# Kernel optimization log

Hardware: AMD Instinct MI355X
Metric: run time of the kernel (lower is better)

The kernel has to match this reference:

```python
import jax, jax.numpy as jnp
import numpy as np

NG, NC, D, E, L, OUT = 100000, 2000, 256, 1000000, 2, 64


def setup_inputs() -> dict:
    key = jax.random.key(0)
    ks = jax.random.split(key, 16)
    s = 1.0 / np.sqrt(D)
    return dict(
        x_gene=jax.random.normal(ks[0], (NG, D), dtype=jnp.float32),
        x_cell=jax.random.normal(ks[1], (NC, D), dtype=jnp.float32),
        src_g2c=jax.random.randint(ks[2], (E,), 0, NG),
        dst_g2c=jax.random.randint(ks[3], (E,), 0, NC),
        src_c2g=jax.random.randint(ks[4], (E,), 0, NC),
        dst_c2g=jax.random.randint(ks[5], (E,), 0, NG),
        idx_gg=jnp.arange(NG),
        idx_cc=jnp.arange(NC),
        w_g2c=jax.random.uniform(ks[6], (E,), dtype=jnp.float32),
        w_c2g=jax.random.uniform(ks[7], (E,), dtype=jnp.float32),
        w_gg=jax.random.uniform(ks[8], (NG,), dtype=jnp.float32),
        w_cc=jax.random.uniform(ks[9], (NC,), dtype=jnp.float32),
        Wrel=jax.random.normal(ks[10], (L, 4, D, D), dtype=jnp.float32) * s,
        brel=jax.random.normal(ks[11], (L, 4, D), dtype=jnp.float32) * 0.1,
        Wroot=jax.random.normal(ks[12], (L, 4, D, D), dtype=jnp.float32) * s,
        Wout=jax.random.normal(ks[13], (OUT, D), dtype=jnp.float32) * s,
        bout=jax.random.normal(ks[14], (OUT,), dtype=jnp.float32) * 0.1,
    )


def _agg(x_src, src, dst, w, n_dst):
    # GraphConv message: x_j * edge_weight, then scatter-add to destinations
    msg = x_src[src] * w[:, None]  # [E, D]
    return jax.ops.segment_sum(msg, dst, num_segments=n_dst)


def reference(x_gene, x_cell, src_g2c, dst_g2c, src_c2g, dst_c2g,
              idx_gg, idx_cc, w_g2c, w_c2g, w_gg, w_cc,
              Wrel, brel, Wroot, Wout, bout):
    xg, xc = x_gene, x_cell
    for l in range(L):
        # relation 0: gene -> cell_type; 1: cell_type -> gene;
        # relation 2: gene self-loop; 3: cell_type self-loop
        agg_c = _agg(xg, src_g2c, dst_g2c, w_g2c, NC)
        agg_g = _agg(xc, src_c2g, dst_c2g, w_c2g, NG)
        agg_gg = _agg(xg, idx_gg, idx_gg, w_gg, NG)
        agg_cc = _agg(xc, idx_cc, idx_cc, w_cc, NC)
        # GraphConv: lin_rel(agg) + bias + lin_root(x_dst); HeteroConv aggr='sum'
        new_c = (agg_c @ Wrel[l, 0].T + brel[l, 0] + xc @ Wroot[l, 0].T
                 + agg_cc @ Wrel[l, 3].T + brel[l, 3] + xc @ Wroot[l, 3].T)
        new_g = (agg_g @ Wrel[l, 1].T + brel[l, 1] + xg @ Wroot[l, 1].T
                 + agg_gg @ Wrel[l, 2].T + brel[l, 2] + xg @ Wroot[l, 2].T)
        xg, xc = jax.nn.relu(new_g), jax.nn.relu(new_c)
    return xc @ Wout.T + bout  # [NC, OUT]
```

## Files before the change

### kernel.cpp

```cpp
#include <hip/hip_runtime.h>

static constexpr int NG   = 100000;
static constexpr int NC   = 2000;
static constexpr int D    = 256;
static constexpr int NE   = 1000000;
static constexpr int NOUTD= 64;
static constexpr int KCAT = 768;

typedef __bf16 bf16x8 __attribute__((ext_vector_type(8)));
typedef float  f32x4  __attribute__((ext_vector_type(4)));

__device__ __forceinline__ unsigned short f2bf(float f) {
    unsigned u = __float_as_uint(f);
    u += 0x7fffu + ((u >> 16) & 1u);
    return (unsigned short)(u >> 16);
}
__device__ __forceinline__ float bflo(unsigned x) { return __uint_as_float((x & 0xffffu) << 16); }
__device__ __forceinline__ float bfhi(unsigned x) { return __uint_as_float(x & 0xffff0000u); }

__device__ __forceinline__ void async16(const void* g, void* l) {
    __builtin_amdgcn_global_load_lds(
        (const __attribute__((address_space(1))) void*)g,
        (__attribute__((address_space(3))) void*)l, 16, 0, 0);
}

__global__ void prep_x(const float* __restrict__ x, const float* __restrict__ w,
                       unsigned short* __restrict__ dx, unsigned short* __restrict__ dv,
                       long stride, int rows) {
    int i = blockIdx.x * blockDim.x + threadIdx.x;
    if (i >= rows * (D / 4)) return;
    int row = i >> 6, c4 = (i & 63) * 4;
    float4 xv = *reinterpret_cast<const float4*>(x + (size_t)row * D + c4);
    float wv = w[row];
    uint2 ox, ov;
    ox.x = (unsigned)f2bf(xv.x) | ((unsigned)f2bf(xv.y) << 16);
    ox.y = (unsigned)f2bf(xv.z) | ((unsigned)f2bf(xv.w) << 16);
    ov.x = (unsigned)f2bf(xv.x * wv) | ((unsigned)f2bf(xv.y * wv) << 16);
    ov.y = (unsigned)f2bf(xv.z * wv) | ((unsigned)f2bf(xv.w * wv) << 16);
    *reinterpret_cast<uint2*>(dx + (size_t)row * stride + c4) = ox;
    *reinterpret_cast<uint2*>(dv + (size_t)row * stride + c4) = ov;
}

__global__ void build_wcat3(const float* __restrict__ Wrel, const float* __restrict__ Wroot,
                            const float* __restrict__ brel,
                            unsigned short* __restrict__ Wg0, unsigned short* __restrict__ Wc0,
                            unsigned short* __restrict__ Wc1,
                            float* __restrict__ bg0, float* __restrict__ bc0,
                            float* __restrict__ bc1) {
    int i = blockIdx.x * blockDim.x + threadIdx.x;
    if (i >= D * D) return;
    int ia, ib; unsigned short* wout; float* bsum;
    if (blockIdx.y == 0)      { ia = 1; ib = 2; wout = Wg0; bsum = bg0; }
    else if (blockIdx.y == 1) { ia = 0; ib = 3; wout = Wc0; bsum = bc0; }
    else                      { ia = 4; ib = 7; wout = Wc1; bsum = bc1; }
    const int WW = D * D;
    int n = i >> 8, k = i & 255;
    wout[(size_t)n * KCAT + k]        = f2bf(Wrel[ia * WW + i]);
    wout[(size_t)n * KCAT + 256 + k]  = f2bf(Wroot[ia * WW + i] + Wroot[ib * WW + i]);
    wout[(size_t)n * KCAT + 512 + k]  = f2bf(Wrel[ib * WW + i]);
    if (i < D) bsum[i] = brel[ia * D + i] + brel[ib * D + i];
}

static constexpr int CC_CHUNK = 8192;
__global__ __launch_bounds__(256) void coarse_count(const int* __restrict__ dst_g2c,
                                                    const int* __restrict__ dst_c2g,
                                                    int* __restrict__ hist) {
    __shared__ int h[512];
    h[threadIdx.x] = 0; h[256 + threadIdx.x] = 0;
    __syncthreads();
    int base = blockIdx.x * CC_CHUNK;
#pragma unroll 4
    for (int t = 0; t < CC_CHUNK / 256; ++t) {
        int e = base + t * 256 + threadIdx.x;
        if (e < NE) {
            atomicAdd(&h[dst_g2c[e] >> 3], 1);
            atomicAdd(&h[256 + (dst_c2g[e] >> 9)], 1);
        }
    }
    __syncthreads();
    if (h[threadIdx.x]) atomicAdd(&hist[threadIdx.x], h[threadIdx.x]);
    if (h[256 + threadIdx.x]) atomicAdd(&hist[256 + threadIdx.x], h[256 + threadIdx.x]);
}

__global__ __launch_bounds__(256) void coarse_scan(const int* __restrict__ hist,
                                                   int* __restrict__ cbase,
                                                   int* __restrict__ ccur_c, int* __restrict__ ccur_g,
                                                   int* __restrict__ rp_c, int* __restrict__ rp_g) {
    __shared__ int sd[256];
    int t = threadIdx.x;
    {
        int v = hist[t];
        sd[t] = v; __syncthreads();
        for (int off = 1; off < 256; off <<= 1) {
            int u = (t >= off) ? sd[t - off] : 0; __syncthreads();
            sd[t] += u; __syncthreads();
        }
        int e = sd[t] - v;
        cbase[t] = e; ccur_c[t] = e;
        if (t == 255) cbase[256] = sd[255];
        __syncthreads();
    }
    {
        int v = hist[256 + t];
        sd[t] = v; __syncthreads();
        for (int off = 1; off < 256; off <<= 1) {
            int u = (t >= off) ? sd[t - off] : 0; __syncthreads();
            sd[t] += u; __syncthreads();
        }
        int e = sd[t] - v;
        cbase[257 + t] = e; ccur_g[t] = e;
        if (t == 255) cbase[513] = sd[255];
    }
    if (t == 0) { rp_c[NC] = NE; rp_g[NG] = NE; }
}

static constexpr int P1_CHUNK = 8192;
__global__ __launch_bounds__(256) void bucket_pass1(
        const int* __restrict__ srcA, const int* __restrict__ dstA, const float* __restrict__ wA,
        int* __restrict__ curA, int2* __restrict__ outA,
        const int* __restrict__ srcB, const int* __restrict__ dstB, const float* __restrict__ wB,
        int* __restrict__ curB, int2* __restrict__ outB) {
    __shared__ int hist[256], lcur[256], gbase[256];
    const int* src; const int* dst; const float* w; int* coarse_cur; int2* out;
    int shift, packshift;
    if (blockIdx.y == 0) { src = srcA; dst = dstA; w = wA; coarse_cur = curA; out = outA; shift = 3; packshift = 17; }
    else { src = srcB; dst = dstB; w = wB; coarse_cur = curB; out = outB; shift = 9; packshift = 11; }
    int tid = threadIdx.x;
    hist[tid] = 0;
    __syncthreads();
    int base = blockIdx.x * P1_CHUNK;
    int mybin[P1_CHUNK / 256];
#pragma unroll
    for (int t = 0; t < P1_CHUNK / 256; ++t) {
        int e = base + t * 256 + tid;
        if (e < NE) {
            int b = dst[e] >> shift;
            mybin[t] = b;
            atomicAdd(&hist[b], 1);
        } else mybin[t] = -1;
    }
    __syncthreads();
    int v = hist[tid];
    gbase[tid] = v ? atomicAdd(&coarse_cur[tid], v) : 0;
    lcur[tid] = 0;
    __syncthreads();
#pragma unroll
    for (int t = 0; t < P1_CHUNK / 256; ++t) {
        int b = mybin[t];
        if (b < 0) continue;
        int e = base + t * 256 + tid;
        int pos = gbase[b] + atomicAdd(&lcur[b], 1);
        int dl = dst[e] & ((1 << shift) - 1);
        out[pos] = make_int2(src[e] | (dl << packshift), __float_as_int(w[e]));
    }
}

static constexpr int P2_CBLK = NC / 8;
static constexpr int P2_GBLK = (NG + 511) / 512;
__global__ __launch_bounds__(256) void bucket_pass2(
        const int2* __restrict__ stC, int2* __restrict__ outC, int* __restrict__ rpC,
        const int2* __restrict__ stG, int2* __restrict__ outG, int* __restrict__ rpG,
        const int* __restrict__ cbase) {
    __shared__ int hist[512], cur[512], sd[256];
    const int2* staged; int2* out; int* rp; const int* cb;
    int shift, packshift, ndst, b;
    if (blockIdx.x < P2_CBLK) {
        staged = stC; out = outC; rp = rpC; cb = cbase;
        shift = 3; packshift = 17; ndst = NC; b = blockIdx.x;
    } else {
        staged = stG; out = outG; rp = rpG; cb = cbase + 257;
        shift = 9; packshift = 11; ndst = NG; b = blockIdx.x - P2_CBLK;
    }
    int tid = threadIdx.x;
    int nf = 1 << shift;
    int d0 = b << shift;
    int j0 = cb[b], j1 = cb[b + 1];
    for (int f = tid; f < nf; f += 256) hist[f] = 0;
    __syncthreads();
    for (int j = j0 + tid; j < j1; j += 256)
        atomicAdd(&hist[((unsigned)staged[j].x) >> packshift], 1);
    __syncthreads();
    int chunk = (nf + 255) >> 8;
    int s = 0;
#pragma unroll 2
    for (int k = 0; k < chunk; ++k) {
        int idx = tid * chunk + k;
        if (idx < nf) s += hist[idx];
    }
    sd[tid] = s; __syncthreads();
    for (int off = 1; off < 256; off <<= 1) {
        int u = (tid >= off) ? sd[tid - off] : 0; __syncthreads();
        sd[tid] += u; __syncthreads();
    }
    int run = sd[tid] - s;
#pragma unroll 2
    for (int k = 0; k < chunk; ++k) {
        int idx = tid * chunk + k;
        if (idx < nf) {
            int h = hist[idx];
            int pos = j0 + run;
            cur[idx] = pos;
            int d = d0 + idx;
            if (d < ndst) rp[d] = pos;
            run += h;
        }
    }
    __syncthreads();
    for (int j = j0 + tid; j < j1; j += 256) {
        int2 e = staged[j];
        int f = ((unsigned)e.x) >> packshift;
        int pos = atomicAdd(&cur[f], 1);
        out[pos] = make_int2(e.x & ((1 << packshift) - 1), e.y);
    }
}

__global__ __launch_bounds__(256) void sort_cell_edges(const int* __restrict__ rp,
                                                       int2* __restrict__ ec) {
    __shared__ int2 s[1024];
    int c = blockIdx.x;
    int j0 = rp[c], j1 = rp[c + 1];
    int n = j1 - j0;
    if (n <= 1 || n > 1024) return;
    for (int i = threadIdx.x; i < 1024; i += 256)
        s[i] = (i < n) ? ec[j0 + i] : make_int2(0x7fffffff, 0);
    __syncthreads();
    for (int k = 2; k <= 1024; k <<= 1) {
        for (int jj = k >> 1; jj > 0; jj >>= 1) {
#pragma unroll
            for (int t = 0; t < 4; ++t) {
                int i = threadIdx.x + t * 256;
                int ixj = i ^ jj;
                if (ixj > i) {
                    int2 a = s[i], b = s[ixj];
                    bool up = ((i & k) == 0);
                    if ((a.x > b.x) == up) { s[i] = b; s[ixj] = a; }
                }
            }
            __syncthreads();
        }
    }
    for (int i = threadIdx.x; i < n; i += 256) ec[j0 + i] = s[i];
}

__global__ void agg_gene_conv(const int* __restrict__ rp, const int2* __restrict__ eg,
                              const unsigned short* __restrict__ src, long sstride,
                              const float* __restrict__ x_gene,
                              unsigned short* __restrict__ xg0b,
                              unsigned short* __restrict__ agg_out, int nrows) {
    int wave = (blockIdx.x * blockDim.x + threadIdx.x) >> 6;
    int lane = threadIdx.x & 63;
    if (wave >= nrows) return;
    float4 xv = *reinterpret_cast<const float4*>(x_gene + (size_t)wave * D + lane * 4);
    uint2 xo;
    xo.x = (unsigned)f2bf(xv.x) | ((unsigned)f2bf(xv.y) << 16);
    xo.y = (unsigned)f2bf(xv.z) | ((unsigned)f2bf(xv.w) << 16);
    *reinterpret_cast<uint2*>(xg0b + (size_t)wave * D + lane * 4) = xo;
    int j0 = __builtin_amdgcn_readfirstlane(rp[wave]);
    int j1 = __builtin_amdgcn_readfirstlane(rp[wave + 1]);
    int half = lane >> 5;
    int lh = lane & 31;
    float a0=0.f,a1=0.f,a2=0.f,a3=0.f,a4=0.f,a5=0.f,a6=0.f,a7=0.f;
    int j = j0;
    for (; j + 4 <= j1; j += 4) {
        int2 e0 = eg[j], e1 = eg[j + 1], e2 = eg[j + 2], e3 = eg[j + 3];
        int   rA = half ? e1.x : e0.x;
        float wA = __int_as_float(half ? e1.y : e0.y);
        int   rB = half ? e3.x : e2.x;
        float wB = __int_as_float(half ? e3.y : e2.y);
        uint4 pA = *reinterpret_cast<const uint4*>(src + (size_t)rA * sstride + lh * 8);
        uint4 pB = *reinterpret_cast<const uint4*>(src + (size_t)rB * sstride + lh * 8);
        a0 += wA * bflo(pA.x) + wB * bflo(pB.x);
        a1 += wA * bfhi(pA.x) + wB * bfhi(pB.x);
        a2 += wA * bflo(pA.y) + wB * bflo(pB.y);
        a3 += wA * bfhi(pA.y) + wB * bfhi(pB.y);
        a4 += wA * bflo(pA.z) + wB * bflo(pB.z);
        a5 += wA * bfhi(pA.z) + wB * bfhi(pB.z);
        a6 += wA * bflo(pA.w) + wB * bflo(pB.w);
        a7 += wA * bfhi(pA.w) + wB * bfhi(pB.w);
    }
    for (; j < j1; j += 2) {
        int2 e0 = eg[j];
        int2 e1 = (j + 1 < j1) ? eg[j + 1] : make_int2(e0.x, 0);
        int   r = half ? e1.x : e0.x;
        float w = __int_as_float(half ? e1.y : e0.y);
        uint4 p = *reinterpret_cast<const uint4*>(src + (size_t)r * sstride + lh * 8);
        a0 += w * bflo(p.x); a1 += w * bfhi(p.x);
        a2 += w * bflo(p.y); a3 += w * bfhi(p.y);
        a4 += w * bflo(p.z); a5 += w * bfhi(p.z);
        a6 += w * bflo(p.w); a7 += w * bfhi(p.w);
    }
    a0 += __shfl_xor(a0, 32, 64); a1 += __shfl_xor(a1, 32, 64);
    a2 += __shfl_xor(a2, 32, 64); a3 += __shfl_xor(a3, 32, 64);
    a4 += __shfl_xor(a4, 32, 64); a5 += __shfl_xor(a5, 32, 64);
    a6 += __shfl_xor(a6, 32, 64); a7 += __shfl_xor(a7, 32, 64);
    if (lane < 32) {
        uint4 o;
        o.x = (unsigned)f2bf(a0) | ((unsigned)f2bf(a1) << 16);
        o.y = (unsigned)f2bf(a2) | ((unsigned)f2bf(a3) << 16);
        o.z = (unsigned)f2bf(a4) | ((unsigned)f2bf(a5) << 16);
        o.w = (unsigned)f2bf(a6) | ((unsigned)f2bf(a7) << 16);
        *reinterpret_cast<uint4*>(agg_out + (size_t)wave * D + lane * 8) = o;
    }
}

__global__ __launch_bounds__(256, 2) void gene_gemm(
        const unsigned short* __restrict__ Agg,
        const unsigned short* __restrict__ Xb,
        const float* __restrict__ w_gg,
        const unsigned short* __restrict__ W,
        const float* __restrict__ bias,
        unsigned short* __restrict__ xg1) {
    __shared__ unsigned short As[128 * 64];
    __shared__ unsigned short Bs1[128 * 64];
    __shared__ unsigned short Bs2[128 * 64];
    int tid = threadIdx.x;
    int wv = tid >> 6, ln = tid & 63;
    int lm = ln & 15, lq = ln >> 4;
    int m0 = blockIdx.x * 128;
    int nb = blockIdx.y * 128;
    int m0w = m0 + (wv >> 1) * 64;
    int n0w = nb + (wv & 1) * 64;

    f32x4 accA[4][4], accV[4][4];
#pragma unroll
    for (int i = 0; i < 4; ++i)
#pragma unroll
        for (int j = 0; j < 4; ++j) { accA[i][j] = f32x4{0,0,0,0}; accV[i][j] = f32x4{0,0,0,0}; }

    for (int k0 = 0; k0 < 256; k0 += 64) {
#pragma unroll
        for (int t = 0; t < 4; ++t) {
            int ci = t * 256 + tid;
            int r = ci >> 3, s = ci & 7;
            int cg = s ^ (r & 7);
            int row = m0 + r; if (row >= NG) row = NG - 1;
            async16(Agg + (size_t)row * D + k0 + cg * 8, (unsigned char*)As + ci * 16);
            async16(W + (size_t)(nb + r) * KCAT + k0 + cg * 8, (unsigned char*)Bs1 + ci * 16);
        }
        __syncthreads();
#pragma unroll
        for (int kk = 0; kk < 2; ++kk) {
            bf16x8 a[4], b[4];
#pragma unroll
            for (int i = 0; i < 4; ++i) {
                int r = (wv >> 1) * 64 + i * 16 + lm;
                int s = (kk * 4 + lq) ^ (r & 7);
                a[i] = *reinterpret_cast<const bf16x8*>(As + (r * 8 + s) * 8);
            }
#pragma unroll
            for (int j = 0; j < 4; ++j) {
                int r = (wv & 1) * 64 + j * 16 + lm;
                int s = (kk * 4 + lq) ^ (r & 7);
                b[j] = *reinterpret_cast<const bf16x8*>(Bs1 + (r * 8 + s) * 8);
            }
#pragma unroll
            for (int i = 0; i < 4; ++i)
#pragma unroll
                for (int j = 0; j < 4; ++j)
                    accA[i][j] = __builtin_amdgcn_mfma_f32_16x16x32_bf16(a[i], b[j], accA[i][j], 0, 0, 0);
        }
        __syncthreads();
    }

    for (int k0 = 0; k0 < 256; k0 += 64) {
#pragma unroll
        for (int t = 0; t < 4; ++t) {
            int ci = t * 256 + tid;
            int r = ci >> 3, s = ci & 7;
            int cg = s ^ (r & 7);
            int row = m0 + r; if (row >= NG) row = NG - 1;
            async16(Xb + (size_t)row * D + k0 + cg * 8, (unsigned char*)As + ci * 16);
            async16(W + (size_t)(nb + r) * KCAT + 256 + k0 + cg * 8, (unsigned char*)Bs1 + ci * 16);
            async16(W + (size_t)(nb + r) * KCAT + 512 + k0 + cg * 8, (unsigned char*)Bs2 + ci * 16);
        }
        __syncthreads();
#pragma unroll
        for (int kk = 0; kk < 2; ++kk) {
            bf16x8 a[4], b1[4], b2[4];
#pragma unroll
            for (int i = 0; i < 4; ++i) {
                int r = (wv >> 1) * 64 + i * 16 + lm;
                int s = (kk * 4 + lq) ^ (r & 7);
                a[i] = *reinterpret_cast<const bf16x8*>(As + (r * 8 + s) * 8);
            }
#pragma unroll
            for (int j = 0; j < 4; ++j) {
                int r = (wv & 1) * 64 + j * 16 + lm;
                int s = (kk * 4 + lq) ^ (r & 7);
                b1[j] = *reinterpret_cast<const bf16x8*>(Bs1 + (r * 8 + s) * 8);
                b2[j] = *reinterpret_cast<const bf16x8*>(Bs2 + (r * 8 + s) * 8);
            }
#pragma unroll
            for (int i = 0; i < 4; ++i)
#pragma unroll
                for (int j = 0; j < 4; ++j) {
                    accA[i][j] = __builtin_amdgcn_mfma_f32_16x16x32_bf16(a[i], b1[j], accA[i][j], 0, 0, 0);
                    accV[i][j] = __builtin_amdgcn_mfma_f32_16x16x32_bf16(a[i], b2[j], accV[i][j], 0, 0, 0);
                }
        }
        __syncthreads();
    }

#pragma unroll
    for (int i = 0; i < 4; ++i) {
#pragma unroll
        for (int r4 = 0; r4 < 4; ++r4) {
            int row = m0w + i * 16 + lq * 4 + r4;
            if (row >= NG) continue;
            float wr = w_gg[row];
#pragma unroll
            for (int j = 0; j < 4; ++j) {
                int col = n0w + j * 16 + lm;
                float v = accA[i][j][r4] + wr * accV[i][j][r4] + bias[col];
                v = v > 0.f ? v : 0.f;
                xg1[(size_t)row * D + col] = f2bf(v);
            }
        }
    }
}

__global__ __launch_bounds__(256) void agg_cell(const int* __restrict__ rp,
                                                const int2* __restrict__ ec,
                                                const unsigned short* __restrict__ src, long sstride,
                                                unsigned short* __restrict__ out, long ostride) {
    __shared__ float red[4][D];
    int c = blockIdx.x;
    int wv = threadIdx.x >> 6, ln = threadIdx.x & 63;
    int j0 = __builtin_amdgcn_readfirstlane(rp[c]);
    int j1 = __builtin_amdgcn_readfirstlane(rp[c + 1]);
    float a0 = 0.f, a1 = 0.f, a2 = 0.f, a3 = 0.f;
    int npair = (j1 - j0) & ~7;
    for (int j = j0 + wv * 2; j < j0 + npair; j += 8) {
        int2 e1 = ec[j], e2 = ec[j + 1];
        float w1 = __int_as_float(e1.y), w2 = __int_as_float(e2.y);
        uint2 p1 = *reinterpret_cast<const uint2*>(src + (size_t)e1.x * sstride + ln * 4);
        uint2 p2 = *reinterpret_cast<const uint2*>(src + (size_t)e2.x * sstride + ln * 4);
        a0 += w1 * bflo(p1.x) + w2 * bflo(p2.x);
        a1 += w1 * bfhi(p1.x) + w2 * bfhi(p2.x);
        a2 += w1 * bflo(p1.y) + w2 * bflo(p2.y);
        a3 += w1 * bfhi(p1.y) + w2 * bfhi(p2.y);
    }
    for (int j = j0 + npair + wv; j < j1; j += 4) {
        int2 e = ec[j];
        float w = __int_as_float(e.y);
        uint2 pk = *reinterpret_cast<const uint2*>(src + (size_t)e.x * sstride + ln * 4);
        a0 += w * bflo(pk.x); a1 += w * bfhi(pk.x);
        a2 += w * bflo(pk.y); a3 += w * bfhi(pk.y);
    }
    red[wv][ln * 4 + 0] = a0; red[wv][ln * 4 + 1] = a1;
    red[wv][ln * 4 + 2] = a2; red[wv][ln * 4 + 3] = a3;
    __syncthreads();
    int col = threadIdx.x;
    float s = red[0][col] + red[1][col] + red[2][col] + red[3][col];
    out[(size_t)c * ostride + col] = f2bf(s);
}

__global__ __launch_bounds__(256, 2) void gemm_tile(
        const unsigned short* __restrict__ A,
        const unsigned short* __restrict__ W,
        const float* __restrict__ bias,
        const float* __restrict__ wrow,
        unsigned short* __restrict__ xout, long xstride,
        unsigned short* __restrict__ vout,
        int M) {
    __shared__ unsigned short As[128 * 64];
    __shared__ unsigned short Bs[128 * 64];
    int tid = threadIdx.x;
    int wv = tid >> 6, ln = tid & 63;
    int lm = ln & 15, lq = ln >> 4;
    int m0 = blockIdx.x * 128;
    int nb = blockIdx.y * 128;
    int m0w = m0 + (wv >> 1) * 64;
    int n0w = nb + (wv & 1) * 64;

    f32x4 acc[4][4];
#pragma unroll
    for (int i = 0; i < 4; ++i)
#pragma unroll
        for (int j = 0; j < 4; ++j) acc[i][j] = f32x4{0.f, 0.f, 0.f, 0.f};

    for (int k0 = 0; k0 < KCAT; k0 += 64) {
#pragma unroll
        for (int t = 0; t < 4; ++t) {
            int ci = t * 256 + tid;
            int r = ci >> 3, s = ci & 7;
            int cg = s ^ (r & 7);
            int row = m0 + r; if (row >= M) row = M - 1;
            async16(A + (size_t)row * KCAT + k0 + cg * 8,
                    (unsigned char*)As + ci * 16);
        }
#pragma unroll
        for (int t = 0; t < 4; ++t) {
            int ci = t * 256 + tid;
            int r = ci >> 3, s = ci & 7;
            int cg = s ^ (r & 7);
            async16(W + (size_t)(nb + r) * KCAT + k0 + cg * 8,
                    (unsigned char*)Bs + ci * 16);
        }
        __syncthreads();
#pragma unroll
        for (int kk = 0; kk < 2; ++kk) {
            bf16x8 a[4], b[4];
#pragma unroll
            for (int i = 0; i < 4; ++i) {
                int r = (wv >> 1) * 64 + i * 16 + lm;
                int c = kk * 4 + lq;
                int s = c ^ (r & 7);
                a[i] = *reinterpret_cast<const bf16x8*>(As + (r * 8 + s) * 8);
            }
#pragma unroll
            for (int j = 0; j < 4; ++j) {
                int r = (wv & 1) * 64 + j * 16 + lm;
                int c = kk * 4 + lq;
                int s = c ^ (r & 7);
                b[j] = *reinterpret_cast<const bf16x8*>(Bs + (r * 8 + s) * 8);
            }
#pragma unroll
            for (int i = 0; i < 4; ++i)
#pragma unroll
                for (int j = 0; j < 4; ++j)
                    acc[i][j] = __builtin_amdgcn_mfma_f32_16x16x32_bf16(a[i], b[j], acc[i][j], 0, 0, 0);
        }
        __syncthreads();
    }

#pragma unroll
    for (int i = 0; i < 4; ++i) {
#pragma unroll
        for (int r4 = 0; r4 < 4; ++r4) {
            int rr = m0w + i * 16 + lq * 4 + r4;
            if (rr >= M) continue;
            float wr = wrow ? wrow[rr] : 0.f;
#pragma unroll
            for (int j = 0; j < 4; ++j) {
                int col = n0w + j * 16 + lm;
                float v = acc[i][j][r4] + bias[col];
                v = v > 0.f ? v : 0.f;
                xout[(size_t)rr * xstride + col] = f2bf(v);
                if (vout) vout[(size_t)rr * xstride + col] = f2bf(v * wr);
            }
        }
    }
}

__global__ void out_kernel(const unsigned short* __restrict__ xc, const float* __restrict__ Wout,
                           const float* __restrict__ bout, float* __restrict__ out) {
    __shared__ float srow[4][D];
    int r = threadIdx.x >> 6;
    int o = threadIdx.x & 63;
    int c = blockIdx.x * 4 + r;
    for (int t = threadIdx.x; t < 4 * D; t += 256) {
        int rr = blockIdx.x * 4 + (t >> 8);
        unsigned short h = xc[(size_t)rr * D + (t & 255)];
        srow[t >> 8][t & 255] = __uint_as_float(((unsigned)h) << 16);
    }
    __syncthreads();
    float s = 0.f;
    const float* wo = Wout + o * D;
    for (int k = 0; k < D; ++k) s += srow[r][k] * wo[k];
    out[(size_t)c * NOUTD + o] = s + bout[o];
}

extern "C" void kernel_launch(void* const* d_in, const int* in_sizes, int n_in,
                              void* d_out, int out_size, void* d_ws, size_t ws_size,
                              hipStream_t stream) {
    const float* x_gene = (const float*)d_in[0];
    const float* x_cell = (const float*)d_in[1];
    const int*   src_g2c = (const int*)d_in[2];
    const int*   dst_g2c = (const int*)d_in[3];
    const int*   src_c2g = (const int*)d_in[4];
    const int*   dst_c2g = (const int*)d_in[5];
    const float* w_g2c = (const float*)d_in[8];
    const float* w_c2g = (const float*)d_in[9];
    const float* w_gg  = (const float*)d_in[10];
    const float* w_cc  = (const float*)d_in[11];
    const float* Wrel  = (const float*)d_in[12];
    const float* brel  = (const float*)d_in[13];
    const float* Wroot = (const float*)d_in[14];
    const float* Wout  = (const float*)d_in[15];
    const float* bout  = (const float*)d_in[16];
    float* out = (float*)d_out;

    char* p = (char*)d_ws;
    auto alloc = [&](size_t bytes) -> char* {
        char* r = p;
        p += (bytes + 255) & ~(size_t)255;
        return r;
    };

    unsigned short* xg0b    = (unsigned short*)alloc((size_t)NG * D * 2);
    unsigned short* xg1     = (unsigned short*)alloc((size_t)NG * D * 2);
    unsigned short* agg_g   = (unsigned short*)alloc((size_t)NG * D * 2);
    unsigned short* Acat_c0 = (unsigned short*)alloc((size_t)NC * KCAT * 2);
    unsigned short* Acat_c1 = (unsigned short*)alloc((size_t)NC * KCAT * 2);
    unsigned short* xc2     = (unsigned short*)alloc((size_t)NC * D * 2);
    int* rp_g  = (int*)alloc((NG + 1) * 4);
    int* rp_c  = (int*)alloc((NC + 1) * 4);
    int2* ec = (int2*)alloc((size_t)NE * 8);
    int2* eg = (int2*)alloc((size_t)NE * 8);
    int2* st_c = (int2*)alloc((size_t)NE * 8);
    int2* st_g = (int2*)alloc((size_t)NE * 8);
    int* hist512 = (int*)alloc(512 * 4);
    int* cbase   = (int*)alloc(514 * 4);
    int* ccur_c  = (int*)alloc(256 * 4);
    int* ccur_g  = (int*)alloc(256 * 4);
    unsigned short* Wg0 = (unsigned short*)alloc((size_t)D * KCAT * 2);
    unsigned short* Wc0 = (unsigned short*)alloc((size_t)D * KCAT * 2);
    unsigned short* Wc1 = (unsigned short*)alloc((size_t)D * KCAT * 2);
    float* bg0 = (float*)alloc(D * 4);
    float* bc0 = (float*)alloc(D * 4);
    float* bc1 = (float*)alloc(D * 4);

    hipMemsetAsync(hist512, 0, 512 * 4, stream);

    prep_x<<<(NC * 64 + 255) / 256, 256, 0, stream>>>(x_cell, w_cc, Acat_c0 + 256, Acat_c0 + 512, KCAT, NC);

    build_wcat3<<<dim3((D * D + 255) / 256, 3), 256, 0, stream>>>(
        Wrel, Wroot, brel, Wg0, Wc0, Wc1, bg0, bc0, bc1);

    coarse_count<<<(NE + CC_CHUNK - 1) / CC_CHUNK, 256, 0, stream>>>(dst_g2c, dst_c2g, hist512);
    coarse_scan<<<1, 256, 0, stream>>>(hist512, cbase, ccur_c, ccur_g, rp_c, rp_g);
    const int P1B = (NE + P1_CHUNK - 1) / P1_CHUNK;
    bucket_pass1<<<dim3(P1B, 2), 256, 0, stream>>>(
        src_g2c, dst_g2c, w_g2c, ccur_c, st_c,
        src_c2g, dst_c2g, w_c2g, ccur_g, st_g);
    bucket_pass2<<<P2_CBLK + P2_GBLK, 256, 0, stream>>>(
        st_c, ec, rp_c, st_g, eg, rp_g, cbase);
    sort_cell_edges<<<NC, 256, 0, stream>>>(rp_c, ec);

    agg_gene_conv<<<(NG + 3) / 4, 256, 0, stream>>>(
        rp_g, eg, Acat_c0 + 256, KCAT, x_gene, xg0b, agg_g, NG);
    gene_gemm<<<dim3((NG + 127) / 128, 2), 256, 0, stream>>>(
        agg_g, xg0b, w_gg, Wg0, bg0, xg1);

    agg_cell<<<NC, 256, 0, stream>>>(rp_c, ec, xg0b, D, Acat_c0, KCAT);
    gemm_tile<<<dim3((NC + 127) / 128, 2), 256, 0, stream>>>(
        Acat_c0, Wc0, bc0, w_cc, Acat_c1 + 256, KCAT, Acat_c1 + 512, NC);

    agg_cell<<<NC, 256, 0, stream>>>(rp_c, ec, xg1, D, Acat_c1, KCAT);
    gemm_tile<<<dim3((NC + 127) / 128, 2), 256, 0, stream>>>(
        Acat_c1, Wc1, bc1, nullptr, xc2, D, nullptr, NC);

    out_kernel<<<NC / 4, 256, 0, stream>>>(xc2, Wout, bout, out);
}
```

Measured before the change: 623.5 us.

## Move x_gene bf16 conversion into coarse_count and tile Wout through LDS

The fp32-to-bf16 conversion of x_gene moves out of the gene aggregation kernel and into extra blocks appended to the coarse histogram kernel. This takes a 100 MB streaming read off the gather-heavy aggregation pass and runs it next to the small histogram work. Separately, out_kernel now handles 8 rows per block and stages Wout into padded LDS in two halves, instead of having each thread read Wout rows from global memory. The conversion blocks add no dependency problems, since xg0b is first read by gene_gemm and agg_cell, which run later.

Measured after the change: 616.1 us. No clear change (-1.2%).

```diff
diff --git a/kernel.cpp b/kernel.cpp
--- a/kernel.cpp
+++ b/kernel.cpp
@@ -62,10 +62,23 @@
 }
 
 static constexpr int CC_CHUNK = 8192;
-__global__ __launch_bounds__(256) void coarse_count(const int* __restrict__ dst_g2c,
-                                                    const int* __restrict__ dst_c2g,
-                                                    int* __restrict__ hist) {
+static constexpr int CCB = (NE + CC_CHUNK - 1) / CC_CHUNK;
+static constexpr int CONVB = NG * (D / 4) / 256;
+__global__ __launch_bounds__(256) void coarse_count_conv(
+        const int* __restrict__ dst_g2c, const int* __restrict__ dst_c2g,
+        int* __restrict__ hist,
+        const float* __restrict__ x_gene, unsigned short* __restrict__ xg0b) {
     __shared__ int h[512];
+    if (blockIdx.x >= CCB) {
+        int i = (blockIdx.x - CCB) * 256 + threadIdx.x;
+        int row = i >> 6, c4 = (i & 63) * 4;
+        float4 xv = *reinterpret_cast<const float4*>(x_gene + (size_t)row * D + c4);
+        uint2 xo;
+        xo.x = (unsigned)f2bf(xv.x) | ((unsigned)f2bf(xv.y) << 16);
+        xo.y = (unsigned)f2bf(xv.z) | ((unsigned)f2bf(xv.w) << 16);
+        *reinterpret_cast<uint2*>(xg0b + (size_t)row * D + c4) = xo;
+        return;
+    }
     h[threadIdx.x] = 0; h[256 + threadIdx.x] = 0;
     __syncthreads();
     int base = blockIdx.x * CC_CHUNK;
@@ -242,19 +255,12 @@
     for (int i = threadIdx.x; i < n; i += 256) ec[j0 + i] = s[i];
 }
 
-__global__ void agg_gene_conv(const int* __restrict__ rp, const int2* __restrict__ eg,
-                              const unsigned short* __restrict__ src, long sstride,
-                              const float* __restrict__ x_gene,
-                              unsigned short* __restrict__ xg0b,
-                              unsigned short* __restrict__ agg_out, int nrows) {
+__global__ void agg_gene(const int* __restrict__ rp, const int2* __restrict__ eg,
+                         const unsigned short* __restrict__ src, long sstride,
+                         unsigned short* __restrict__ agg_out, int nrows) {
     int wave = (blockIdx.x * blockDim.x + threadIdx.x) >> 6;
     int lane = threadIdx.x & 63;
     if (wave >= nrows) return;
-    float4 xv = *reinterpret_cast<const float4*>(x_gene + (size_t)wave * D + lane * 4);
-    uint2 xo;
-    xo.x = (unsigned)f2bf(xv.x) | ((unsigned)f2bf(xv.y) << 16);
-    xo.y = (unsigned)f2bf(xv.z) | ((unsigned)f2bf(xv.w) << 16);
-    *reinterpret_cast<uint2*>(xg0b + (size_t)wave * D + lane * 4) = xo;
     int j0 = __builtin_amdgcn_readfirstlane(rp[wave]);
     int j1 = __builtin_amdgcn_readfirstlane(rp[wave + 1]);
     int half = lane >> 5;
@@ -543,22 +549,37 @@
     }
 }
 
-__global__ void out_kernel(const unsigned short* __restrict__ xc, const float* __restrict__ Wout,
-                           const float* __restrict__ bout, float* __restrict__ out) {
-    __shared__ float srow[4][D];
-    int r = threadIdx.x >> 6;
-    int o = threadIdx.x & 63;
-    int c = blockIdx.x * 4 + r;
-    for (int t = threadIdx.x; t < 4 * D; t += 256) {
-        int rr = blockIdx.x * 4 + (t >> 8);
+__global__ __launch_bounds__(256) void out_kernel(const unsigned short* __restrict__ xc,
+                                                  const float* __restrict__ Wout,
+                                                  const float* __restrict__ bout,
+                                                  float* __restrict__ out) {
+    __shared__ float srow[8][D];
+    __shared__ float wlds[32][D + 1];
+    int tid = threadIdx.x;
+    for (int t = tid; t < 8 * D; t += 256) {
+        int rr = blockIdx.x * 8 + (t >> 8);
         unsigned short h = xc[(size_t)rr * D + (t & 255)];
         srow[t >> 8][t & 255] = __uint_as_float(((unsigned)h) << 16);
     }
-    __syncthreads();
-    float s = 0.f;
-    const float* wo = Wout + o * D;
-    for (int k = 0; k < D; ++k) s += srow[r][k] * wo[k];
-    out[(size_t)c * NOUTD + o] = s + bout[o];
+    int r = tid >> 5, ol = tid & 31;
+    float res[2];
+#pragma unroll
+    for (int p = 0; p < 2; ++p) {
+        __syncthreads();
+        for (int t = tid; t < 32 * (D / 4); t += 256) {
+            int o = t >> 6, k4 = (t & 63) * 4;
+            float4 wv = *reinterpret_cast<const float4*>(Wout + (size_t)(p * 32 + o) * D + k4);
+            wlds[o][k4 + 0] = wv.x; wlds[o][k4 + 1] = wv.y;
+            wlds[o][k4 + 2] = wv.z; wlds[o][k4 + 3] = wv.w;
+        }
+        __syncthreads();
+        float s = 0.f;
+        for (int k = 0; k < D; ++k) s += srow[r][k] * wlds[ol][k];
+        res[p] = s;
+    }
+    int c = blockIdx.x * 8 + r;
+    out[(size_t)c * NOUTD + ol] = res[0] + bout[ol];
+    out[(size_t)c * NOUTD + 32 + ol] = res[1] + bout[32 + ol];
 }
 
 extern "C" void kernel_launch(void* const* d_in, const int* in_sizes, int n_in,
@@ -618,7 +639,7 @@
     build_wcat3<<<dim3((D * D + 255) / 256, 3), 256, 0, stream>>>(
         Wrel, Wroot, brel, Wg0, Wc0, Wc1, bg0, bc0, bc1);
 
-    coarse_count<<<(NE + CC_CHUNK - 1) / CC_CHUNK, 256, 0, stream>>>(dst_g2c, dst_c2g, hist512);
+    coarse_count_conv<<<CCB + CONVB, 256, 0, stream>>>(dst_g2c, dst_c2g, hist512, x_gene, xg0b);
     coarse_scan<<<1, 256, 0, stream>>>(hist512, cbase, ccur_c, ccur_g, rp_c, rp_g);
     const int P1B = (NE + P1_CHUNK - 1) / P1_CHUNK;
     bucket_pass1<<<dim3(P1B, 2), 256, 0, stream>>>(
@@ -628,8 +649,8 @@
         st_c, ec, rp_c, st_g, eg, rp_g, cbase);
     sort_cell_edges<<<NC, 256, 0, stream>>>(rp_c, ec);
 
-    agg_gene_conv<<<(NG + 3) / 4, 256, 0, stream>>>(
-        rp_g, eg, Acat_c0 + 256, KCAT, x_gene, xg0b, agg_g, NG);
+    agg_gene<<<(NG + 3) / 4, 256, 0, stream>>>(
+        rp_g, eg, Acat_c0 + 256, KCAT, agg_g, NG);
     gene_gemm<<<dim3((NG + 127) / 128, 2), 256, 0, stream>>>(
         agg_g, xg0b, w_gg, Wg0, bg0, xg1);
 
@@ -641,5 +662,5 @@
     gemm_tile<<<dim3((NC + 127) / 128, 2), 256, 0, stream>>>(
         Acat_c1, Wc1, bc1, nullptr, xc2, D, nullptr, NC);
 
-    out_kernel<<<NC / 4, 256, 0, stream>>>(xc2, Wout, bout, out);
-}
+    out_kernel<<<NC / 8, 256, 0, stream>>>(xc2, Wout, bout, out);
+}
```
